# Optimization experiments

Measured on AMD Instinct MI355X. Metric: run time of the kernel, lower is better.

The kernel has to match this reference:

```python
import jax, jax.numpy as jnp
import numpy as np

N_NODES = 25000
N_EDGES = 300000
N_GRAPHS = 256
EMB_DIM = 92
HID = 256
EDGE_F = 4


def _lin(key, fan_in, fan_out):
    kw, kb = jax.random.split(key)
    s = 1.0 / np.sqrt(fan_in)
    W = jax.random.uniform(kw, (fan_in, fan_out), jnp.float32, -s, s)
    b = jax.random.uniform(kb, (fan_out,), jnp.float32, -s, s)
    return W, b


def setup_inputs() -> dict:
    key = jax.random.key(0)
    ks = jax.random.split(key, 32)
    x_atoms = jax.random.randint(ks[0], (N_NODES,), 0, 119)
    edge_index = jax.random.randint(ks[1], (2, N_EDGES), 0, N_NODES)
    edge_attr = jax.random.normal(ks[2], (N_EDGES, EDGE_F), jnp.float32)
    batch = jnp.sort(jax.random.randint(ks[3], (N_NODES,), 0, N_GRAPHS))
    emb = jax.random.normal(ks[4], (119, EMB_DIM), jnp.float32)
    emb = emb.at[0].set(0.0)  # padding_idx=0
    # layer 0: in=92, out=256
    ew1_0, eb1_0 = _lin(ks[5], EDGE_F, EMB_DIM)
    ew2_0, eb2_0 = _lin(ks[6], EMB_DIM, EMB_DIM)
    nw_0, nb_0 = _lin(ks[7], EMB_DIM, HID)
    # layers 1..3 stacked: in=out=256
    ew1, eb1, ew2, eb2, nw, nb = [], [], [], [], [], []
    for i in range(3):
        a, b = _lin(ks[8 + 3 * i], EDGE_F, HID)
        c, d = _lin(ks[9 + 3 * i], HID, HID)
        e, f = _lin(ks[10 + 3 * i], HID, HID)
        ew1.append(a); eb1.append(b); ew2.append(c); eb2.append(d); nw.append(e); nb.append(f)
    ew1 = jnp.stack(ew1); eb1 = jnp.stack(eb1); ew2 = jnp.stack(ew2)
    eb2 = jnp.stack(eb2); nw = jnp.stack(nw); nb = jnp.stack(nb)
    rw1, rb1 = _lin(ks[20], HID, HID)
    rw2, rb2 = _lin(ks[21], HID, HID // 2)
    rw3, rb3 = _lin(ks[22], HID // 2, 1)
    return dict(x_atoms=x_atoms, edge_index=edge_index, edge_attr=edge_attr, batch=batch,
                emb=emb, ew1_0=ew1_0, eb1_0=eb1_0, ew2_0=ew2_0, eb2_0=eb2_0, nw_0=nw_0, nb_0=nb_0,
                ew1=ew1, eb1=eb1, ew2=ew2, eb2=eb2, nw=nw, nb=nb,
                rw1=rw1, rb1=rb1, rw2=rw2, rb2=rb2, rw3=rw3, rb3=rb3)


def _conv(x, src, dst, edge_attr, ew1, eb1, ew2, eb2, nw, nb):
    # edge MLP: Linear -> Softplus -> Linear
    ee = jax.nn.softplus(edge_attr @ ew1 + eb1) @ ew2 + eb2  # [E, C]
    msg = ee * x[src]                                        # gather + multiply
    agg = jax.ops.segment_sum(msg, dst, num_segments=x.shape[0])  # scatter-add
    return jax.nn.softplus(agg @ nw + nb)


def reference(x_atoms, edge_index, edge_attr, batch, emb,
              ew1_0, eb1_0, ew2_0, eb2_0, nw_0, nb_0,
              ew1, eb1, ew2, eb2, nw, nb,
              rw1, rb1, rw2, rb2, rw3, rb3):
    src, dst = edge_index[0], edge_index[1]  # PyG: x_j = x[src], aggregate at dst
    x = emb[x_atoms]  # [N, 92]
    x = _conv(x, src, dst, edge_attr, ew1_0, eb1_0, ew2_0, eb2_0, nw_0, nb_0)
    for i in range(3):
        x = _conv(x, src, dst, edge_attr, ew1[i], eb1[i], ew2[i], eb2[i], nw[i], nb[i])
    # global mean pool
    sums = jax.ops.segment_sum(x, batch, num_segments=N_GRAPHS)
    cnts = jax.ops.segment_sum(jnp.ones((x.shape[0],), x.dtype), batch, num_segments=N_GRAPHS)
    g = sums / jnp.maximum(cnts, 1.0)[:, None]  # [G, 256]
    h = jax.nn.softplus(g @ rw1 + rb1)          # dropout is identity in eval mode
    h = jax.nn.softplus(h @ rw2 + rb2)
    out = (h @ rw3 + rb3).squeeze(-1)           # [G]
    return out
```

## Files before the change

kernel.cpp:

```cpp
#include <hip/hip_runtime.h>
#include <math.h>

#define N_NODES  25000
#define N_EDGES  300000
#define N_GRAPHS 256
#define EMB_DIM  92
#define HID      256

typedef short bf16x8 __attribute__((ext_vector_type(8)));
typedef float f32x4  __attribute__((ext_vector_type(4)));

__device__ __forceinline__ float softplusf(float x){
    return fmaxf(x, 0.0f) + __logf(1.0f + __expf(-fabsf(x)));
}
__device__ __forceinline__ unsigned short f2bf(float f){
    unsigned int u = __float_as_uint(f);
    unsigned int r = (u + 0x7FFFu + ((u >> 16) & 1u)) >> 16;
    return (unsigned short)r;
}
__device__ __forceinline__ unsigned short f2bf_trunc(float f){
    return (unsigned short)(__float_as_uint(f) >> 16);
}
__device__ __forceinline__ float bf2f(unsigned short b){
    return __uint_as_float(((unsigned int)b) << 16);
}
__device__ __forceinline__ void split_bf(float h, unsigned short& hi, unsigned short& lo){
    const unsigned int u = __float_as_uint(h);
    hi = (unsigned short)(u >> 16);
    const float r = h - __uint_as_float(u & 0xFFFF0000u);
    lo = (unsigned short)(__float_as_uint(r) >> 16);
}
__device__ __forceinline__ int xcd_window(int nwin){
    const int per = (nwin + 7) >> 3;
    const int win = (blockIdx.x & 7) * per + (blockIdx.x >> 3);
    return (win < nwin) ? win : -1;
}

__global__ void gather_emb_kernel(const int* __restrict__ atoms,
                                  const float* __restrict__ emb,
                                  float* __restrict__ x)
{
    const int n = blockIdx.x;
    const int c = threadIdx.x;
    if (c < EMB_DIM){
        const int a = atoms[n];
        x[(size_t)n*EMB_DIM + c] = emb[(size_t)a*EMB_DIM + c];
    }
}

__global__ __launch_bounds__(256) void hist_kernel(const int* __restrict__ dst, int* __restrict__ hist,
                                                   const int* __restrict__ batch, int* __restrict__ gcnt){
    const int e = blockIdx.x*256 + threadIdx.x;
    if (e < N_EDGES) atomicAdd(&hist[dst[e]], 1);
    if (e < N_NODES) atomicAdd(&gcnt[batch[e]], 1);
}

__global__ __launch_bounds__(1024) void scan_kernel(const int* __restrict__ hist, int* __restrict__ cursor){
    __shared__ int chunk[1024];
    const int t = threadIdx.x;
    const int base = t*25;
    int local[25];
    int s = 0;
    #pragma unroll
    for (int i=0;i<25;i++){
        const int idx = base+i;
        const int v = (idx < N_NODES) ? hist[idx] : 0;
        local[i] = s; s += v;
    }
    chunk[t] = s;
    __syncthreads();
    for (int off=1; off<1024; off<<=1){
        int v = (t >= off) ? chunk[t-off] : 0;
        __syncthreads();
        chunk[t] += v;
        __syncthreads();
    }
    const int pre = (t > 0) ? chunk[t-1] : 0;
    #pragma unroll
    for (int i=0;i<25;i++){
        const int idx = base+i;
        if (idx < N_NODES) cursor[idx] = pre + local[i];
    }
}

__global__ __launch_bounds__(256) void scatter_kernel(const int* __restrict__ src, const int* __restrict__ dst,
                                                      const float* __restrict__ ea,
                                                      int* __restrict__ cursor,
                                                      int* __restrict__ src_s, int* __restrict__ dst_s,
                                                      float* __restrict__ ea_s){
    const int e = blockIdx.x*256 + threadIdx.x;
    if (e < N_EDGES){
        const int d = dst[e];
        const int pos = atomicAdd(&cursor[d], 1);
        src_s[pos] = src[e];
        dst_s[pos] = d;
        const float4 a = *(const float4*)(ea + (size_t)e*4);
        *(float4*)(ea_s + (size_t)pos*4) = a;
    }
}

__device__ __forceinline__ void pack256_dev(const float* w, unsigned short* whi, unsigned short* wlo, int f){
    const int layer = f >> 7;
    const int rem   = f & 127;
    const int ntile = rem >> 3;
    const int k8    = rem & 7;
    for (int i = threadIdx.x; i < 512; i += 256){
        const int lane = i >> 3, j = i & 7;
        const int k = k8*32 + (lane >> 4)*8 + j;
        const int n = ntile*16 + (lane & 15);
        const float v = w[(size_t)layer*HID*HID + (size_t)k*HID + n];
        const unsigned short hb = f2bf(v);
        whi[(size_t)f*512 + i] = hb;
        wlo[(size_t)f*512 + i] = f2bf(v - bf2f(hb));
    }
}
__device__ __forceinline__ void packpad_dev(const float* w, int Kin, int Nin, int ldn,
                                            unsigned short* whi, unsigned short* wlo, int f){
    const int k8 = f % 3;
    const int ntile = f / 3;
    for (int i = threadIdx.x; i < 512; i += 256){
        const int lane = i >> 3, j = i & 7;
        const int k = k8*32 + (lane >> 4)*8 + j;
        const int n = ntile*16 + (lane & 15);
        float v = 0.0f;
        if (k < Kin && n < Nin) v = w[(size_t)k*ldn + n];
        const unsigned short hb = f2bf(v);
        whi[(size_t)f*512 + i] = hb;
        wlo[(size_t)f*512 + i] = f2bf(v - bf2f(hb));
    }
}
__global__ __launch_bounds__(256) void pack_all_kernel(
    const float* __restrict__ ew2, const float* __restrict__ nw,
    const float* __restrict__ ew2_0, const float* __restrict__ nw_0,
    unsigned short* whi, unsigned short* wlo,
    unsigned short* nwhi, unsigned short* nwlo,
    unsigned short* w92hi, unsigned short* w92lo,
    unsigned short* nw92hi, unsigned short* nw92lo)
{
    const int b = blockIdx.x;
    if (b < 384)      pack256_dev(ew2, whi, wlo, b);
    else if (b < 768) pack256_dev(nw, nwhi, nwlo, b-384);
    else if (b < 786) packpad_dev(ew2_0, EMB_DIM, EMB_DIM, EMB_DIM, w92hi, w92lo, b-768);
    else              packpad_dev(nw_0, EMB_DIM, HID, HID, nw92hi, nw92lo, b-786);
}

__global__ __launch_bounds__(256, 4) void edge_conv92_mfma_kernel(
    const int* __restrict__ src_s, const int* __restrict__ dst_s,
    const float* __restrict__ ea_s,
    const float* __restrict__ w1, const float* __restrict__ b1,
    const unsigned short* __restrict__ whi, const unsigned short* __restrict__ wlo,
    const float* __restrict__ b2,
    const float* __restrict__ x92, float* __restrict__ agg92)
{
    constexpr int C = EMB_DIM;
    constexpr int KP = 96;
    constexpr int LDA = 104;
    constexpr int EPB = 64;
    constexpr int NWIN = (N_EDGES + EPB - 1) / EPB;
    __shared__ unsigned short aHi[EPB][LDA];
    __shared__ float eaS[EPB][4];
    __shared__ int   srcS[EPB];
    __shared__ int   dstS[EPB];

    const int win = xcd_window(NWIN);
    if (win < 0) return;
    const int e0  = win * EPB;
    const int tid = threadIdx.x;

    {
        const int e = tid >> 2, comp = tid & 3;
        const int eid = min(e0 + e, N_EDGES-1);
        eaS[e][comp] = ea_s[(size_t)eid*4 + comp];
        if (tid < EPB){
            const int eid2 = min(e0 + tid, N_EDGES-1);
            srcS[tid] = src_s[eid2];
            dstS[tid] = dst_s[eid2];
        }
    }
    __syncthreads();

    for (int idx = tid; idx < EPB*KP; idx += 256){
        const int e = idx / KP, k = idx - e*KP;
        float h = 0.0f;
        if (k < C){
            const float4 a = *(const float4*)&eaS[e][0];
            h = softplusf(fmaf(a.x, w1[k], fmaf(a.y, w1[C+k],
                          fmaf(a.z, w1[2*C+k], fmaf(a.w, w1[3*C+k], b1[k])))));
        }
        const int row = (e>>5)*32 + ((e>>2)&1)*16 + ((e>>3)&3)*4 + (e&3);
        aHi[row][k] = f2bf_trunc(h);
    }
    __syncthreads();

    const int lane = tid & 63, wv = tid >> 6;
    const int quad = lane >> 4, fcol = lane & 15;
    const int mpair = wv >> 1;
    const int ngrp  = wv & 1;

    f32x4 acc[2][3];
    #pragma unroll
    for (int m=0;m<2;m++)
        #pragma unroll
        for (int t=0;t<3;t++)
            #pragma unroll
            for (int j=0;j<4;j++) acc[m][t][j] = 0.0f;

    for (int k8=0;k8<3;k8++){
        bf16x8 ah[2];
        #pragma unroll
        for (int m=0;m<2;m++)
            ah[m] = *(const bf16x8*)(&aHi[mpair*32 + m*16 + fcol][0] + k8*32 + quad*8);
        #pragma unroll
        for (int t=0;t<3;t++){
            const int fi = (ngrp*3 + t)*3 + k8;
            const bf16x8 bh = *(const bf16x8*)(whi + (size_t)fi*512 + lane*8);
            const bf16x8 bl = *(const bf16x8*)(wlo + (size_t)fi*512 + lane*8);
            #pragma unroll
            for (int m=0;m<2;m++){
                acc[m][t] = __builtin_amdgcn_mfma_f32_16x16x32_bf16(ah[m], bh, acc[m][t], 0, 0, 0);
                acc[m][t] = __builtin_amdgcn_mfma_f32_16x16x32_bf16(ah[m], bl, acc[m][t], 0, 0, 0);
            }
        }
    }

    int   ncol[3]; float bb[3];
    #pragma unroll
    for (int t=0;t<3;t++){
        ncol[t] = (ngrp*3 + t)*16 + fcol;
        bb[t] = (ncol[t] < C) ? b2[ncol[t]] : 0.0f;
    }

    const int ebase = mpair*32 + quad*8;
    float xv[8][3];
    #pragma unroll
    for (int j=0;j<8;j++){
        const int s = srcS[ebase + j];
        const bool valid = (e0 + ebase + j) < N_EDGES;
        #pragma unroll
        for (int t=0;t<3;t++)
            xv[j][t] = (valid && ncol[t] < C) ? x92[(size_t)s*C + ncol[t]] : 0.0f;
    }

    int dprev = dstS[ebase];
    float run[3] = {0.f,0.f,0.f};
    #pragma unroll
    for (int j=0;j<8;j++){
        const int d = dstS[ebase + j];
        if (d != dprev){
            #pragma unroll
            for (int t=0;t<3;t++){
                if (ncol[t] < C) atomicAdd(&agg92[(size_t)dprev*C + ncol[t]], run[t]);
                run[t] = 0.0f;
            }
            dprev = d;
        }
        #pragma unroll
        for (int t=0;t<3;t++)
            run[t] += (acc[j>>2][t][j&3] + bb[t]) * xv[j][t];
    }
    #pragma unroll
    for (int t=0;t<3;t++)
        if (ncol[t] < C) atomicAdd(&agg92[(size_t)dprev*C + ncol[t]], run[t]);
}

__global__ __launch_bounds__(256) void node_update92_mfma_kernel(
    const float* __restrict__ agg92,
    const unsigned short* __restrict__ whi, const unsigned short* __restrict__ wlo,
    const float* __restrict__ b, float* __restrict__ xout)
{
    constexpr int C = EMB_DIM;
    constexpr int KP = 96;
    constexpr int LDA = 104;
    __shared__ unsigned short aHi[16][LDA];
    __shared__ unsigned short aLo[16][LDA];

    const int n0  = blockIdx.x * 16;
    const int tid = threadIdx.x;

    for (int idx = tid; idx < 16*KP; idx += 256){
        const int i = idx / KP, k = idx - i*KP;
        const int node = n0 + i;
        float v = 0.0f;
        if (k < C && node < N_NODES) v = agg92[(size_t)node*C + k];
        unsigned short hb, lb;
        split_bf(v, hb, lb);
        aHi[i][k] = hb;
        aLo[i][k] = lb;
    }
    __syncthreads();

    const int lane = tid & 63, wv = tid >> 6;
    const int quad = lane >> 4, fcol = lane & 15;

    f32x4 acc[4];
    #pragma unroll
    for (int t=0;t<4;t++)
        #pragma unroll
        for (int j=0;j<4;j++) acc[t][j] = 0.0f;

    const unsigned short* aHrow = &aHi[fcol][0];
    const unsigned short* aLrow = &aLo[fcol][0];

    for (int k8=0;k8<3;k8++){
        const bf16x8 ah = *(const bf16x8*)(aHrow + k8*32 + quad*8);
        const bf16x8 al = *(const bf16x8*)(aLrow + k8*32 + quad*8);
        #pragma unroll
        for (int t=0;t<4;t++){
            const int fi = (wv*4 + t)*3 + k8;
            const bf16x8 bh = *(const bf16x8*)(whi + (size_t)fi*512 + lane*8);
            const bf16x8 bl = *(const bf16x8*)(wlo + (size_t)fi*512 + lane*8);
            acc[t] = __builtin_amdgcn_mfma_f32_16x16x32_bf16(ah, bh, acc[t], 0, 0, 0);
            acc[t] = __builtin_amdgcn_mfma_f32_16x16x32_bf16(ah, bl, acc[t], 0, 0, 0);
            acc[t] = __builtin_amdgcn_mfma_f32_16x16x32_bf16(al, bh, acc[t], 0, 0, 0);
        }
    }

    #pragma unroll
    for (int i=0;i<4;i++){
        const int node = n0 + quad*4 + i;
        if (node < N_NODES){
            #pragma unroll
            for (int t=0;t<4;t++){
                const int n = (wv*4 + t)*16 + fcol;
                xout[(size_t)node*HID + n] = softplusf(acc[t][i] + b[n]);
            }
        }
    }
}

__global__ __launch_bounds__(512, 6) void edge_conv256_mfma_kernel(
    const int* __restrict__ src_s, const int* __restrict__ dst_s,
    const float* __restrict__ ea_s,
    const float* __restrict__ w1, const float* __restrict__ b1,
    const unsigned short* __restrict__ whi,
    const float* __restrict__ b2,
    const float* __restrict__ x, float* __restrict__ agg)
{
    constexpr int C = HID;
    constexpr int LDA = C + 8;
    constexpr int EPB = 64;
    constexpr int NWIN = (N_EDGES + EPB - 1) / EPB;
    __shared__ unsigned short aHi[EPB][LDA];
    __shared__ float eaS[EPB][4];
    __shared__ int   srcS[EPB];
    __shared__ int   dstS[EPB];

    const int win = xcd_window(NWIN);
    if (win < 0) return;
    const int e0  = win * EPB;
    const int tid = threadIdx.x;

    if (tid < 256){
        const int e = tid >> 2, comp = tid & 3;
        const int eid = min(e0 + e, N_EDGES-1);
        eaS[e][comp] = ea_s[(size_t)eid*4 + comp];
    } else if (tid < 320){
        const int e = tid - 256;
        srcS[e] = src_s[min(e0 + e, N_EDGES-1)];
    } else if (tid < 384){
        const int e = tid - 320;
        dstS[e] = dst_s[min(e0 + e, N_EDGES-1)];
    }
    __syncthreads();

    {
        const int k2 = (tid & 127) * 2;
        const int g  = tid >> 7;
        const float wa0 = w1[k2],   wa1 = w1[C+k2],   wa2 = w1[2*C+k2],   wa3 = w1[3*C+k2];
        const float wb0 = w1[k2+1], wb1 = w1[C+k2+1], wb2 = w1[2*C+k2+1], wb3 = w1[3*C+k2+1];
        const float bk0 = b1[k2], bk1 = b1[k2+1];
        #pragma unroll
        for (int ii=0; ii<16; ii++){
            const int e = g*16 + ii;
            const float4 a = *(const float4*)&eaS[e][0];
            const float v0 = fmaf(a.x,wa0,fmaf(a.y,wa1,fmaf(a.z,wa2,fmaf(a.w,wa3,bk0))));
            const float v1 = fmaf(a.x,wb0,fmaf(a.y,wb1,fmaf(a.z,wb2,fmaf(a.w,wb3,bk1))));
            const unsigned int packed = (unsigned int)f2bf_trunc(softplusf(v0))
                                      | ((unsigned int)f2bf_trunc(softplusf(v1)) << 16);
            const int q = e >> 4, j = e & 15;
            *(unsigned int*)&aHi[(j>>2)*16 + q*4 + (j&3)][k2] = packed;
        }
    }
    __syncthreads();

    const int lane = tid & 63, wv = tid >> 6;
    const int quad = lane >> 4, fcol = lane & 15;

    f32x4 acc[4][2];
    #pragma unroll
    for (int m=0;m<4;m++)
        #pragma unroll
        for (int t=0;t<2;t++)
            #pragma unroll
            for (int j=0;j<4;j++) acc[m][t][j] = 0.0f;

    for (int k8=0;k8<8;k8++){
        bf16x8 ah[4];
        #pragma unroll
        for (int m=0;m<4;m++)
            ah[m] = *(const bf16x8*)(&aHi[m*16 + fcol][0] + k8*32 + quad*8);
        #pragma unroll
        for (int t=0;t<2;t++){
            const int fi = (wv*2 + t)*8 + k8;
            const bf16x8 bh = *(const bf16x8*)(whi + (size_t)fi*512 + lane*8);
            #pragma unroll
            for (int m=0;m<4;m++)
                acc[m][t] = __builtin_amdgcn_mfma_f32_16x16x32_bf16(ah[m], bh, acc[m][t], 0, 0, 0);
        }
    }

    float bb[2];
    #pragma unroll
    for (int t=0;t<2;t++) bb[t] = b2[(wv*2 + t)*16 + fcol];

    const int ebase = quad*16;
    float xv[16][2];
    #pragma unroll
    for (int j=0;j<16;j++){
        const int s = srcS[ebase + j];
        const bool valid = (e0 + ebase + j) < N_EDGES;
        #pragma unroll
        for (int t=0;t<2;t++)
            xv[j][t] = valid ? x[(size_t)s*C + (wv*2 + t)*16 + fcol] : 0.0f;
    }

    int dprev = dstS[ebase];
    float run[2] = {0.f,0.f};
    #pragma unroll
    for (int j=0;j<16;j++){
        const int d = dstS[ebase + j];
        if (d != dprev){
            #pragma unroll
            for (int t=0;t<2;t++){
                atomicAdd(&agg[(size_t)dprev*C + (wv*2 + t)*16 + fcol], run[t]);
                run[t] = 0.0f;
            }
            dprev = d;
        }
        #pragma unroll
        for (int t=0;t<2;t++)
            run[t] += (acc[j>>2][t][j&3] + bb[t]) * xv[j][t];
    }
    #pragma unroll
    for (int t=0;t<2;t++)
        atomicAdd(&agg[(size_t)dprev*C + (wv*2 + t)*16 + fcol], run[t]);
}

__global__ __launch_bounds__(256) void node_update_mfma_kernel(
    float* __restrict__ agg,
    const unsigned short* __restrict__ whi, const unsigned short* __restrict__ wlo,
    const float* __restrict__ b, float* __restrict__ xout, int zero_agg)
{
    constexpr int C = HID;
    constexpr int LDA = C + 8;
    __shared__ unsigned short aHi[16][LDA];
    __shared__ unsigned short aLo[16][LDA];

    const int n0  = blockIdx.x * 16;
    const int tid = threadIdx.x;

    #pragma unroll
    for (int it=0; it<16; it++){
        const int node = n0 + it;
        float v = 0.0f;
        if (node < N_NODES){
            v = agg[(size_t)node*C + tid];
            if (zero_agg) agg[(size_t)node*C + tid] = 0.0f;
        }
        unsigned short hb, lb;
        split_bf(v, hb, lb);
        aHi[it][tid] = hb;
        aLo[it][tid] = lb;
    }
    __syncthreads();

    const int lane = tid & 63, wv = tid >> 6;
    const int quad = lane >> 4, fcol = lane & 15;

    f32x4 acc[4];
    #pragma unroll
    for (int t=0;t<4;t++)
        #pragma unroll
        for (int j=0;j<4;j++) acc[t][j] = 0.0f;

    const unsigned short* aHrow = &aHi[fcol][0];
    const unsigned short* aLrow = &aLo[fcol][0];

    for (int k8=0;k8<8;k8++){
        const bf16x8 ah = *(const bf16x8*)(aHrow + k8*32 + quad*8);
        const bf16x8 al = *(const bf16x8*)(aLrow + k8*32 + quad*8);
        #pragma unroll
        for (int t=0;t<4;t++){
            const int fi = (wv*4 + t)*8 + k8;
            const bf16x8 bh = *(const bf16x8*)(whi + (size_t)fi*512 + lane*8);
            const bf16x8 bl = *(const bf16x8*)(wlo + (size_t)fi*512 + lane*8);
            acc[t] = __builtin_amdgcn_mfma_f32_16x16x32_bf16(ah, bh, acc[t], 0, 0, 0);
            acc[t] = __builtin_amdgcn_mfma_f32_16x16x32_bf16(ah, bl, acc[t], 0, 0, 0);
            acc[t] = __builtin_amdgcn_mfma_f32_16x16x32_bf16(al, bh, acc[t], 0, 0, 0);
        }
    }

    #pragma unroll
    for (int i=0;i<4;i++){
        const int node = n0 + quad*4 + i;
        if (node < N_NODES){
            #pragma unroll
            for (int t=0;t<4;t++){
                const int n = (wv*4 + t)*16 + fcol;
                xout[(size_t)node*C + n] = softplusf(acc[t][i] + b[n]);
            }
        }
    }
}

__global__ __launch_bounds__(256) void pool_kernel(
    const float* __restrict__ x, const int* __restrict__ batch,
    float* __restrict__ sums)
{
    constexpr int NPB = 32;
    const int n0 = blockIdx.x * NPB;
    const int c  = threadIdx.x;
    int gprev = batch[n0];
    float run = 0.0f;
    for (int i=0;i<NPB;i++){
        const int n = n0 + i;
        if (n >= N_NODES) break;
        const int g = batch[n];
        if (g != gprev){
            atomicAdd(&sums[(size_t)gprev*HID + c], run);
            run = 0.0f; gprev = g;
        }
        run += x[(size_t)n*HID + c];
    }
    atomicAdd(&sums[(size_t)gprev*HID + c], run);
}

__global__ __launch_bounds__(256) void readout_kernel(
    const float* __restrict__ sums, const int* __restrict__ gcnt,
    const float* __restrict__ rw1, const float* __restrict__ rb1,
    const float* __restrict__ rw2, const float* __restrict__ rb2,
    const float* __restrict__ rw3, const float* __restrict__ rb3,
    float* __restrict__ out)
{
    __shared__ float g[HID];
    __shared__ float h[HID];
    __shared__ float h2[HID/2];
    __shared__ float red[256];
    const int gi = blockIdx.x;
    const int t  = threadIdx.x;
    const float cnt = fmaxf((float)gcnt[gi], 1.0f);
    g[t] = sums[(size_t)gi*HID + t] / cnt;
    __syncthreads();
    float acc = rb1[t];
    for (int k=0;k<HID;k++) acc = fmaf(g[k], rw1[(size_t)k*HID + t], acc);
    h[t] = softplusf(acc);
    __syncthreads();
    if (t < HID/2){
        float a2 = rb2[t];
        for (int k=0;k<HID;k++) a2 = fmaf(h[k], rw2[(size_t)k*(HID/2) + t], a2);
        h2[t] = softplusf(a2);
    }
    __syncthreads();
    red[t] = (t < HID/2) ? h2[t]*rw3[t] : 0.0f;
    __syncthreads();
    for (int s2=128; s2>0; s2>>=1){
        if (t < s2) red[t] += red[t+s2];
        __syncthreads();
    }
    if (t == 0) out[gi] = red[0] + rb3[0];
}

extern "C" void kernel_launch(void* const* d_in, const int* in_sizes, int n_in,
                              void* d_out, int out_size, void* d_ws, size_t ws_size,
                              hipStream_t stream)
{
    const int*   x_atoms = (const int*)d_in[0];
    const int*   eidx    = (const int*)d_in[1];
    const int*   src     = eidx;
    const int*   dst     = eidx + N_EDGES;
    const float* ea      = (const float*)d_in[2];
    const int*   batch   = (const int*)d_in[3];
    const float* emb     = (const float*)d_in[4];
    const float* ew1_0   = (const float*)d_in[5];
    const float* eb1_0   = (const float*)d_in[6];
    const float* ew2_0   = (const float*)d_in[7];
    const float* eb2_0   = (const float*)d_in[8];
    const float* nw_0    = (const float*)d_in[9];
    const float* nb_0    = (const float*)d_in[10];
    const float* ew1     = (const float*)d_in[11];
    const float* eb1     = (const float*)d_in[12];
    const float* ew2     = (const float*)d_in[13];
    const float* eb2     = (const float*)d_in[14];
    const float* nw      = (const float*)d_in[15];
    const float* nb      = (const float*)d_in[16];
    const float* rw1     = (const float*)d_in[17];
    const float* rb1     = (const float*)d_in[18];
    const float* rw2     = (const float*)d_in[19];
    const float* rb2     = (const float*)d_in[20];
    const float* rw3     = (const float*)d_in[21];
    const float* rb3     = (const float*)d_in[22];
    float* out = (float*)d_out;

    float* x    = (float*)d_ws;
    float* agg  = x   + (size_t)N_NODES*HID;
    float* sums = agg + (size_t)N_NODES*HID;
    unsigned short* whi  = (unsigned short*)(sums + (size_t)N_GRAPHS*HID);
    unsigned short* wlo  = whi  + (size_t)3*128*512;
    unsigned short* nwhi = wlo  + (size_t)3*128*512;
    unsigned short* nwlo = nwhi + (size_t)3*128*512;
    unsigned short* w92hi  = nwlo  + (size_t)3*128*512;
    unsigned short* w92lo  = w92hi + (size_t)18*512;
    unsigned short* nw92hi = w92lo + (size_t)18*512;
    unsigned short* nw92lo = nw92hi + (size_t)48*512;
    float* ea_s = (float*)(nw92lo + (size_t)48*512);
    int* hist   = (int*)(ea_s + (size_t)N_EDGES*4);
    int* gcnt   = hist   + N_NODES;
    int* cursor = gcnt   + N_GRAPHS;
    int* src_s  = cursor + N_NODES;
    int* dst_s  = src_s  + N_EDGES;

    hipMemsetAsync(hist, 0, (N_NODES + N_GRAPHS)*sizeof(int), stream);
    hipLaunchKernelGGL(hist_kernel, dim3((N_EDGES+255)/256), dim3(256), 0, stream, dst, hist, batch, gcnt);
    hipLaunchKernelGGL(scan_kernel, dim3(1), dim3(1024), 0, stream, hist, cursor);
    hipLaunchKernelGGL(scatter_kernel, dim3((N_EDGES+255)/256), dim3(256), 0, stream,
                       src, dst, ea, cursor, src_s, dst_s, ea_s);

    hipLaunchKernelGGL(pack_all_kernel, dim3(834), dim3(256), 0, stream,
                       ew2, nw, ew2_0, nw_0,
                       whi, wlo, nwhi, nwlo, w92hi, w92lo, nw92hi, nw92lo);

    const int NWIN64 = (N_EDGES + 63) / 64;

    hipLaunchKernelGGL(gather_emb_kernel, dim3(N_NODES), dim3(128), 0, stream, x_atoms, emb, x);
    hipMemsetAsync(agg, 0, (size_t)N_NODES*EMB_DIM*sizeof(float), stream);
    hipLaunchKernelGGL(edge_conv92_mfma_kernel, dim3((NWIN64+7)/8*8), dim3(256), 0, stream,
                       src_s, dst_s, ea_s, ew1_0, eb1_0, w92hi, w92lo, eb2_0, x, agg);
    hipLaunchKernelGGL(node_update92_mfma_kernel, dim3((N_NODES+15)/16), dim3(256), 0, stream,
                       agg, nw92hi, nw92lo, nb_0, x);

    hipMemsetAsync(agg, 0, (size_t)N_NODES*HID*sizeof(float), stream);

    for (int i=0;i<3;i++){
        hipLaunchKernelGGL(edge_conv256_mfma_kernel, dim3((NWIN64+7)/8*8), dim3(512), 0, stream,
                           src_s, dst_s, ea_s,
                           ew1 + (size_t)i*4*HID, eb1 + (size_t)i*HID,
                           whi + (size_t)i*128*512,
                           eb2 + (size_t)i*HID,
                           x, agg);
        hipLaunchKernelGGL(node_update_mfma_kernel, dim3((N_NODES+15)/16), dim3(256), 0, stream,
                           agg, nwhi + (size_t)i*128*512, nwlo + (size_t)i*128*512,
                           nb + (size_t)i*HID, x, (i < 2) ? 1 : 0);
    }

    hipMemsetAsync(sums, 0, (size_t)N_GRAPHS*HID*sizeof(float), stream);
    hipLaunchKernelGGL(pool_kernel, dim3((N_NODES+31)/32), dim3(256), 0, stream, x, batch, sums);
    hipLaunchKernelGGL(readout_kernel, dim3(N_GRAPHS), dim3(256), 0, stream,
                       sums, gcnt, rw1, rb1, rw2, rb2, rw3, rb3, out);
}
```

Baseline: 656.7 us.

## Fold memsets and pooling into neighbouring kernels, use polynomial softplus

Removes the separate hipMemsetAsync calls by zeroing the hist, gcnt, sums and agg buffers inside existing kernels. The layer-0 aggregation buffer moves to the tail of the full agg region, and the full agg is cleared in the node_update92 kernel. The global mean-pool kernel is fused into the last node update, which accumulates per-graph sums with atomics from registers. Softplus's log1p is replaced by a degree-5 polynomial in exp(-|x|), trading some accuracy for fewer transcendental instructions.

```diff
diff --git a/kernel.cpp b/kernel.cpp
--- a/kernel.cpp
+++ b/kernel.cpp
@@ -11,7 +11,10 @@
 typedef float f32x4  __attribute__((ext_vector_type(4)));
 
 __device__ __forceinline__ float softplusf(float x){
-    return fmaxf(x, 0.0f) + __logf(1.0f + __expf(-fabsf(x)));
+    const float u = __expf(-fabsf(x));
+    const float p = u*fmaf(u, fmaf(u, fmaf(u, fmaf(u, 0.03215845f, -0.13606275f),
+                                            0.28947478f), -0.49190896f), 0.99949556f);
+    return fmaxf(x, 0.0f) + p;
 }
 __device__ __forceinline__ unsigned short f2bf(float f){
     unsigned int u = __float_as_uint(f);
@@ -38,10 +41,16 @@
 
 __global__ void gather_emb_kernel(const int* __restrict__ atoms,
                                   const float* __restrict__ emb,
-                                  float* __restrict__ x)
+                                  float* __restrict__ x,
+                                  int* __restrict__ hist, int* __restrict__ gcnt,
+                                  float* __restrict__ sums)
 {
     const int n = blockIdx.x;
     const int c = threadIdx.x;
+    const int flat = n*128 + c;
+    if (flat < N_NODES) hist[flat] = 0;
+    if (flat < N_GRAPHS) gcnt[flat] = 0;
+    if (flat < N_GRAPHS*HID) sums[flat] = 0.0f;
     if (c < EMB_DIM){
         const int a = atoms[n];
         x[(size_t)n*EMB_DIM + c] = emb[(size_t)a*EMB_DIM + c];
@@ -87,7 +96,8 @@
                                                       const float* __restrict__ ea,
                                                       int* __restrict__ cursor,
                                                       int* __restrict__ src_s, int* __restrict__ dst_s,
-                                                      float* __restrict__ ea_s){
+                                                      float* __restrict__ ea_s,
+                                                      float* __restrict__ agg92){
     const int e = blockIdx.x*256 + threadIdx.x;
     if (e < N_EDGES){
         const int d = dst[e];
@@ -97,6 +107,9 @@
         const float4 a = *(const float4*)(ea + (size_t)e*4);
         *(float4*)(ea_s + (size_t)pos*4) = a;
     }
+    const int nth = gridDim.x*256;
+    for (int i = blockIdx.x*256 + threadIdx.x; i < N_NODES*EMB_DIM; i += nth)
+        agg92[i] = 0.0f;
 }
 
 __device__ __forceinline__ void pack256_dev(const float* w, unsigned short* whi, unsigned short* wlo, int f){
@@ -264,7 +277,8 @@
 }
 
 __global__ __launch_bounds__(256) void node_update92_mfma_kernel(
-    const float* __restrict__ agg92,
+    float* __restrict__ agg92,
+    float* __restrict__ aggfull,
     const unsigned short* __restrict__ whi, const unsigned short* __restrict__ wlo,
     const float* __restrict__ b, float* __restrict__ xout)
 {
@@ -281,7 +295,10 @@
         const int i = idx / KP, k = idx - i*KP;
         const int node = n0 + i;
         float v = 0.0f;
-        if (k < C && node < N_NODES) v = agg92[(size_t)node*C + k];
+        if (k < C && node < N_NODES){
+            v = agg92[(size_t)node*C + k];
+            agg92[(size_t)node*C + k] = 0.0f;
+        }
         unsigned short hb, lb;
         split_bf(v, hb, lb);
         aHi[i][k] = hb;
@@ -326,6 +343,10 @@
             }
         }
     }
+
+    const int nth = gridDim.x*256;
+    for (int idx = blockIdx.x*256 + tid; idx < N_NODES*164; idx += nth)
+        aggfull[idx] = 0.0f;
 }
 
 __global__ __launch_bounds__(512, 6) void edge_conv256_mfma_kernel(
@@ -449,15 +470,19 @@
 __global__ __launch_bounds__(256) void node_update_mfma_kernel(
     float* __restrict__ agg,
     const unsigned short* __restrict__ whi, const unsigned short* __restrict__ wlo,
-    const float* __restrict__ b, float* __restrict__ xout, int zero_agg)
+    const float* __restrict__ b, float* __restrict__ xout, int zero_agg,
+    const int* __restrict__ batch, float* __restrict__ sums, int do_pool)
 {
     constexpr int C = HID;
     constexpr int LDA = C + 8;
     __shared__ unsigned short aHi[16][LDA];
     __shared__ unsigned short aLo[16][LDA];
+    __shared__ int batchS[16];
 
     const int n0  = blockIdx.x * 16;
     const int tid = threadIdx.x;
+
+    if (tid < 16) batchS[tid] = batch[min(n0 + tid, N_NODES-1)];
 
     #pragma unroll
     for (int it=0; it<16; it++){
@@ -500,39 +525,43 @@
         }
     }
 
+    float vals[4][4];
     #pragma unroll
     for (int i=0;i<4;i++){
         const int node = n0 + quad*4 + i;
-        if (node < N_NODES){
-            #pragma unroll
-            for (int t=0;t<4;t++){
+        #pragma unroll
+        for (int t=0;t<4;t++){
+            float v = 0.0f;
+            if (node < N_NODES){
                 const int n = (wv*4 + t)*16 + fcol;
-                xout[(size_t)node*C + n] = softplusf(acc[t][i] + b[n]);
+                v = softplusf(acc[t][i] + b[n]);
+                xout[(size_t)node*C + n] = v;
             }
-        }
-    }
-}
-
-__global__ __launch_bounds__(256) void pool_kernel(
-    const float* __restrict__ x, const int* __restrict__ batch,
-    float* __restrict__ sums)
-{
-    constexpr int NPB = 32;
-    const int n0 = blockIdx.x * NPB;
-    const int c  = threadIdx.x;
-    int gprev = batch[n0];
-    float run = 0.0f;
-    for (int i=0;i<NPB;i++){
-        const int n = n0 + i;
-        if (n >= N_NODES) break;
-        const int g = batch[n];
-        if (g != gprev){
-            atomicAdd(&sums[(size_t)gprev*HID + c], run);
-            run = 0.0f; gprev = g;
-        }
-        run += x[(size_t)n*HID + c];
-    }
-    atomicAdd(&sums[(size_t)gprev*HID + c], run);
+            vals[i][t] = v;
+        }
+    }
+
+    if (do_pool){
+        int gprev = batchS[quad*4];
+        float run[4] = {0.f,0.f,0.f,0.f};
+        #pragma unroll
+        for (int i=0;i<4;i++){
+            const int g = batchS[quad*4 + i];
+            if (g != gprev){
+                #pragma unroll
+                for (int t=0;t<4;t++){
+                    atomicAdd(&sums[(size_t)gprev*HID + (wv*4+t)*16 + fcol], run[t]);
+                    run[t] = 0.0f;
+                }
+                gprev = g;
+            }
+            #pragma unroll
+            for (int t=0;t<4;t++) run[t] += vals[i][t];
+        }
+        #pragma unroll
+        for (int t=0;t<4;t++)
+            atomicAdd(&sums[(size_t)gprev*HID + (wv*4+t)*16 + fcol], run[t]);
+    }
 }
 
 __global__ __launch_bounds__(256) void readout_kernel(
@@ -603,6 +632,7 @@
 
     float* x    = (float*)d_ws;
     float* agg  = x   + (size_t)N_NODES*HID;
+    float* agg92 = agg + (size_t)N_NODES*164;
     float* sums = agg + (size_t)N_NODES*HID;
     unsigned short* whi  = (unsigned short*)(sums + (size_t)N_GRAPHS*HID);
     unsigned short* wlo  = whi  + (size_t)3*128*512;
@@ -619,26 +649,22 @@
     int* src_s  = cursor + N_NODES;
     int* dst_s  = src_s  + N_EDGES;
 
-    hipMemsetAsync(hist, 0, (N_NODES + N_GRAPHS)*sizeof(int), stream);
+    const int NWIN64 = (N_EDGES + 63) / 64;
+
+    hipLaunchKernelGGL(gather_emb_kernel, dim3(N_NODES), dim3(128), 0, stream,
+                       x_atoms, emb, x, hist, gcnt, sums);
     hipLaunchKernelGGL(hist_kernel, dim3((N_EDGES+255)/256), dim3(256), 0, stream, dst, hist, batch, gcnt);
     hipLaunchKernelGGL(scan_kernel, dim3(1), dim3(1024), 0, stream, hist, cursor);
     hipLaunchKernelGGL(scatter_kernel, dim3((N_EDGES+255)/256), dim3(256), 0, stream,
-                       src, dst, ea, cursor, src_s, dst_s, ea_s);
-
+                       src, dst, ea, cursor, src_s, dst_s, ea_s, agg92);
     hipLaunchKernelGGL(pack_all_kernel, dim3(834), dim3(256), 0, stream,
                        ew2, nw, ew2_0, nw_0,
                        whi, wlo, nwhi, nwlo, w92hi, w92lo, nw92hi, nw92lo);
 
-    const int NWIN64 = (N_EDGES + 63) / 64;
-
-    hipLaunchKernelGGL(gather_emb_kernel, dim3(N_NODES), dim3(128), 0, stream, x_atoms, emb, x);
-    hipMemsetAsync(agg, 0, (size_t)N_NODES*EMB_DIM*sizeof(float), stream);
     hipLaunchKernelGGL(edge_conv92_mfma_kernel, dim3((NWIN64+7)/8*8), dim3(256), 0, stream,
-                       src_s, dst_s, ea_s, ew1_0, eb1_0, w92hi, w92lo, eb2_0, x, agg);
+                       src_s, dst_s, ea_s, ew1_0, eb1_0, w92hi, w92lo, eb2_0, x, agg92);
     hipLaunchKernelGGL(node_update92_mfma_kernel, dim3((N_NODES+15)/16), dim3(256), 0, stream,
-                       agg, nw92hi, nw92lo, nb_0, x);
-
-    hipMemsetAsync(agg, 0, (size_t)N_NODES*HID*sizeof(float), stream);
+                       agg92, agg, nw92hi, nw92lo, nb_0, x);
 
     for (int i=0;i<3;i++){
         hipLaunchKernelGGL(edge_conv256_mfma_kernel, dim3((NWIN64+7)/8*8), dim3(512), 0, stream,
@@ -649,11 +675,10 @@
                            x, agg);
         hipLaunchKernelGGL(node_update_mfma_kernel, dim3((N_NODES+15)/16), dim3(256), 0, stream,
                            agg, nwhi + (size_t)i*128*512, nwlo + (size_t)i*128*512,
-                           nb + (size_t)i*HID, x, (i < 2) ? 1 : 0);
-    }
-
-    hipMemsetAsync(sums, 0, (size_t)N_GRAPHS*HID*sizeof(float), stream);
-    hipLaunchKernelGGL(pool_kernel, dim3((N_NODES+31)/32), dim3(256), 0, stream, x, batch, sums);
+                           nb + (size_t)i*HID, x, (i < 2) ? 1 : 0,
+                           batch, sums, (i == 2) ? 1 : 0);
+    }
+
     hipLaunchKernelGGL(readout_kernel, dim3(N_GRAPHS), dim3(256), 0, stream,
                        sums, gcnt, rw1, rb1, rw2, rb2, rw3, rb3, out);
 }
```

After: 648.2 us. No clear change (-1.3%).
